# Kernel tuning notes

Measured on AMD Instinct MI355X. Metric: run time of the kernel, lower is better.

## Reference

```python
import jax, jax.numpy as jnp
import numpy as np

B, T, C, F = 2, 2048, 2048, 8192
LN_EPS = 1e-5


def setup_inputs() -> dict:
    key = jax.random.key(0)
    ks = jax.random.split(key, 24)
    rn = lambda k, s, sc=1.0: jax.random.normal(k, s, jnp.float32) * sc
    un = lambda k, s: jax.random.uniform(k, s, jnp.float32)
    inp = {}
    inp['x'] = rn(ks[0], (B, T, C))
    inp['att_shift'] = rn(ks[1], (B, C))
    # wkv_state rows: aa (num), bb (den), pp (running max exponent)
    inp['wkv_state'] = jnp.stack([jnp.zeros((B, C)), jnp.zeros((B, C)),
                                  jnp.full((B, C), -1e38)], axis=1)
    inp['ffn_shift'] = rn(ks[2], (B, C))
    inp['ln1_g'] = jnp.ones(C); inp['ln1_b'] = jnp.zeros(C)
    inp['ln2_g'] = jnp.ones(C); inp['ln2_b'] = jnp.zeros(C)
    inp['tmk'] = un(ks[3], (C,)); inp['tmv'] = un(ks[4], (C,)); inp['tmr'] = un(ks[5], (C,))
    inp['time_decay'] = rn(ks[6], (C,), 0.5)
    inp['time_first'] = rn(ks[7], (C,), 0.5)
    inp['Wk'] = rn(ks[8], (C, C), 0.02); inp['Wv'] = rn(ks[9], (C, C), 0.02)
    inp['Wr'] = rn(ks[10], (C, C), 0.02); inp['Wo'] = rn(ks[11], (C, C), 0.02)
    inp['fmk'] = un(ks[12], (C,)); inp['fmr'] = un(ks[13], (C,))
    inp['Fk'] = rn(ks[14], (C, F), 0.02)
    inp['Fr'] = rn(ks[15], (C, C), 0.02)
    inp['Fv'] = rn(ks[16], (F, C), 0.02)
    return inp


def layer_norm(x, g, b):
    m = jnp.mean(x, axis=-1, keepdims=True)
    v = jnp.mean(jnp.square(x - m), axis=-1, keepdims=True)
    return (x - m) * jax.lax.rsqrt(v + LN_EPS) * g + b


def wkv(w, u, k, v, state):
    # w: -exp(time_decay) [C], u: time_first [C]; k,v: [B,T,C]; state: [B,3,C]
    def step(carry, kv_t):
        aa, bb, pp = carry
        kt, vt = kv_t
        ww = u + kt
        p = jnp.maximum(pp, ww)
        e1 = jnp.exp(pp - p)
        e2 = jnp.exp(ww - p)
        y = (e1 * aa + e2 * vt) / (e1 * bb + e2)
        ww2 = pp + w
        p2 = jnp.maximum(ww2, kt)
        e1b = jnp.exp(ww2 - p2)
        e2b = jnp.exp(kt - p2)
        return (e1b * aa + e2b * vt, e1b * bb + e2b, p2), y
    carry0 = (state[:, 0], state[:, 1], state[:, 2])
    (aa, bb, pp), ys = jax.lax.scan(step, carry0,
                                    (k.transpose(1, 0, 2), v.transpose(1, 0, 2)))
    return ys.transpose(1, 0, 2), jnp.stack([aa, bb, pp], axis=1)


def reference(x, att_shift, wkv_state, ffn_shift, ln1_g, ln1_b, ln2_g, ln2_b,
              tmk, tmv, tmr, time_decay, time_first, Wk, Wv, Wr, Wo,
              fmk, fmr, Fk, Fr, Fv):
    # ---- time-mix (attention) ----
    x1 = layer_norm(x, ln1_g, ln1_b)
    xx = jnp.concatenate([att_shift[:, None, :], x1[:, :-1]], axis=1)
    xk = x1 * tmk + xx * (1.0 - tmk)
    xv = x1 * tmv + xx * (1.0 - tmv)
    xr = x1 * tmr + xx * (1.0 - tmr)
    k = jnp.einsum('btc,cd->btd', xk, Wk)
    v = jnp.einsum('btc,cd->btd', xv, Wv)
    r = jnp.einsum('btc,cd->btd', xr, Wr)
    y, new_wkv = wkv(-jnp.exp(time_decay), time_first, k, v, wkv_state)
    x = x + jnp.einsum('btd,dc->btc', jax.nn.sigmoid(r) * y, Wo)
    # ---- channel-mix (FFN) ----
    x2 = layer_norm(x, ln2_g, ln2_b)
    xx2 = jnp.concatenate([ffn_shift[:, None, :], x2[:, :-1]], axis=1)
    xk2 = x2 * fmk + xx2 * (1.0 - fmk)
    xr2 = x2 * fmr + xx2 * (1.0 - fmr)
    kf = jnp.square(jax.nn.relu(jnp.einsum('btc,cf->btf', xk2, Fk)))
    kv = jnp.einsum('btf,fc->btc', kf, Fv)
    x = x + jax.nn.sigmoid(jnp.einsum('btc,cd->btd', xr2, Fr)) * kv
    return x, x1[:, -1], new_wkv, x2[:, -1]
```

## Files before the change

kernel.cpp:

```cpp
#include <hip/hip_runtime.h>
#include <stdint.h>

#define B_ 2
#define T_ 2048
#define C_ 2048
#define F_ 8192
#define M_ 4096
#define BC_ 4096
#define CHB 16
#define TCH 16
#define LC2 128

typedef __attribute__((ext_vector_type(8))) __bf16 bf16x8;
typedef __attribute__((ext_vector_type(4))) float f32x4;

__device__ __forceinline__ unsigned short f2bf(float f) {
  union { float f; unsigned u; } v; v.f = f;
  unsigned r = v.u + 0x7fffu + ((v.u >> 16) & 1u);
  return (unsigned short)(r >> 16);
}
__device__ __forceinline__ float b2f(unsigned short h) {
  union { unsigned u; float f; } v; v.u = ((unsigned)h) << 16; return v.f;
}

__device__ __forceinline__ void gload16(const void* g, void* l) {
  __builtin_amdgcn_global_load_lds((__attribute__((address_space(1))) void*)g,
                                   (__attribute__((address_space(3))) void*)l,
                                   16, 0, 0);
}

__global__ __launch_bounds__(256) void k_transpose_cast(
    const float* __restrict__ W, unsigned short* __restrict__ WT, int K, int N) {
  __shared__ unsigned short tile[32][33];
  const int n0 = blockIdx.x * 32, k0 = blockIdx.y * 32;
  const int tx = threadIdx.x & 31, ty = threadIdx.x >> 5;
#pragma unroll
  for (int i = 0; i < 4; ++i)
    tile[ty + 8 * i][tx] = f2bf(W[(size_t)(k0 + ty + 8 * i) * N + n0 + tx]);
  __syncthreads();
#pragma unroll
  for (int i = 0; i < 4; ++i)
    WT[(size_t)(n0 + ty + 8 * i) * K + k0 + tx] = tile[tx][ty + 8 * i];
}

__global__ __launch_bounds__(256) void k_layernorm(
    const float* __restrict__ x, const float* __restrict__ g,
    const float* __restrict__ beta, unsigned short* __restrict__ y,
    float* __restrict__ last_out) {
  const int row = blockIdx.x;
  const int t = row & (T_ - 1);
  const int bi = row >> 11;
  const float* xr = x + (size_t)row * C_;
  const int base = threadIdx.x * 8;
  float lv[8];
  {
    float4 a = *(const float4*)(xr + base);
    float4 b = *(const float4*)(xr + base + 4);
    lv[0]=a.x; lv[1]=a.y; lv[2]=a.z; lv[3]=a.w; lv[4]=b.x; lv[5]=b.y; lv[6]=b.z; lv[7]=b.w;
  }
  float s = 0.f, q = 0.f;
#pragma unroll
  for (int j = 0; j < 8; ++j) { s += lv[j]; q += lv[j] * lv[j]; }
#pragma unroll
  for (int o = 32; o > 0; o >>= 1) { s += __shfl_down(s, o); q += __shfl_down(q, o); }
  __shared__ float rs[4], rq[4];
  if ((threadIdx.x & 63) == 0) { rs[threadIdx.x >> 6] = s; rq[threadIdx.x >> 6] = q; }
  __syncthreads();
  s = rs[0] + rs[1] + rs[2] + rs[3];
  q = rq[0] + rq[1] + rq[2] + rq[3];
  const float mean = s * (1.f / C_);
  const float var = q * (1.f / C_) - mean * mean;
  const float inv = 1.f / sqrtf(var + 1e-5f);
  float ov[8];
  unsigned short o8[8];
#pragma unroll
  for (int j = 0; j < 8; ++j) {
    ov[j] = (lv[j] - mean) * inv * g[base + j] + beta[base + j];
    o8[j] = f2bf(ov[j]);
  }
  *(uint4*)(y + (size_t)row * C_ + base) = *(uint4*)o8;
  if (last_out != nullptr && t == T_ - 1) {
    float* lp = last_out + (size_t)bi * C_ + base;
    *(float4*)lp = make_float4(ov[0], ov[1], ov[2], ov[3]);
    *(float4*)(lp + 4) = make_float4(ov[4], ov[5], ov[6], ov[7]);
  }
}

__global__ __launch_bounds__(256) void k_mix3(
    const unsigned short* __restrict__ x1, const float* __restrict__ shift,
    const float* __restrict__ tmk, const float* __restrict__ tmv,
    const float* __restrict__ tmr,
    unsigned short* __restrict__ xk, unsigned short* __restrict__ xv,
    unsigned short* __restrict__ xr) {
  const int row = blockIdx.x;
  const int t = row & (T_ - 1);
  const int bi = row >> 11;
  const int c0 = threadIdx.x * 8;
  const size_t o = (size_t)row * C_ + c0;
  unsigned short cur8[8];
  *(uint4*)cur8 = *(const uint4*)(x1 + o);
  float pv[8];
  if (t == 0) {
    const float* sp = shift + (size_t)bi * C_ + c0;
#pragma unroll
    for (int j = 0; j < 8; ++j) pv[j] = sp[j];
  } else {
    unsigned short p8[8];
    *(uint4*)p8 = *(const uint4*)(x1 + o - C_);
#pragma unroll
    for (int j = 0; j < 8; ++j) pv[j] = b2f(p8[j]);
  }
  unsigned short ok[8], ov[8], orr[8];
#pragma unroll
  for (int j = 0; j < 8; ++j) {
    const float a = b2f(cur8[j]), p = pv[j];
    const float mk = tmk[c0 + j], mv = tmv[c0 + j], mr = tmr[c0 + j];
    ok[j]  = f2bf(a * mk + p * (1.f - mk));
    ov[j]  = f2bf(a * mv + p * (1.f - mv));
    orr[j] = f2bf(a * mr + p * (1.f - mr));
  }
  *(uint4*)(xk + o) = *(uint4*)ok;
  *(uint4*)(xv + o) = *(uint4*)ov;
  *(uint4*)(xr + o) = *(uint4*)orr;
}

__global__ __launch_bounds__(256) void k_mix2(
    const unsigned short* __restrict__ x2, const float* __restrict__ shift,
    const float* __restrict__ fmk, const float* __restrict__ fmr,
    unsigned short* __restrict__ xk2, unsigned short* __restrict__ xr2) {
  const int row = blockIdx.x;
  const int t = row & (T_ - 1);
  const int bi = row >> 11;
  const int c0 = threadIdx.x * 8;
  const size_t o = (size_t)row * C_ + c0;
  unsigned short cur8[8];
  *(uint4*)cur8 = *(const uint4*)(x2 + o);
  float pv[8];
  if (t == 0) {
    const float* sp = shift + (size_t)bi * C_ + c0;
#pragma unroll
    for (int j = 0; j < 8; ++j) pv[j] = sp[j];
  } else {
    unsigned short p8[8];
    *(uint4*)p8 = *(const uint4*)(x2 + o - C_);
#pragma unroll
    for (int j = 0; j < 8; ++j) pv[j] = b2f(p8[j]);
  }
  unsigned short ok[8], orr[8];
#pragma unroll
  for (int j = 0; j < 8; ++j) {
    const float a = b2f(cur8[j]), p = pv[j];
    const float mk = fmk[c0 + j], mr = fmr[c0 + j];
    ok[j]  = f2bf(a * mk + p * (1.f - mk));
    orr[j] = f2bf(a * mr + p * (1.f - mr));
  }
  *(uint4*)(xk2 + o) = *(uint4*)ok;
  *(uint4*)(xr2 + o) = *(uint4*)orr;
}

__global__ __launch_bounds__(256) void k_wkv_blk(
    const float* __restrict__ kk, const float* __restrict__ vv,
    const float* __restrict__ td, const float* __restrict__ tf,
    const float* __restrict__ st, float* __restrict__ y,
    float* __restrict__ out_state) {
  __shared__ float sA[TCH][CHB], sB[TCH][CHB], sP[TCH][CHB];
  const int blk = blockIdx.x;
  const int bi = blk >> 7;
  const int tx = threadIdx.x & 15;
  const int ty = threadIdx.x >> 4;
  const int c = ((blk & 127) * CHB) + tx;
  const float w = -expf(td[c]);
  const float u = tf[c];
  const size_t base = (size_t)bi * T_ * C_ + (size_t)ty * LC2 * C_ + c;
  const float* kp = kk + base;
  const float* vp = vv + base;
  float aa = 0.f, bb = 0.f, pp = -1e38f;
#pragma unroll 8
  for (int i = 0; i < LC2; ++i) {
    const float kt = kp[(size_t)i * C_], vt = vp[(size_t)i * C_];
    const float ww2 = pp + w;
    const float p2 = fmaxf(ww2, kt);
    const float e1b = expf(ww2 - p2), e2b = expf(kt - p2);
    aa = e1b * aa + e2b * vt;
    bb = e1b * bb + e2b;
    pp = p2;
  }
  sA[ty][tx] = aa; sB[ty][tx] = bb; sP[ty][tx] = pp;
  __syncthreads();
  if (ty == 0) {
    const float* s0 = st + (size_t)bi * 3 * C_;
    float ca = s0[c], cb = s0[C_ + c], cp = s0[2 * C_ + c];
    const float wL = w * (float)LC2;
#pragma unroll
    for (int j = 0; j < TCH; ++j) {
      const float a2 = sA[j][tx], b2 = sB[j][tx], p2 = sP[j][tx];
      sA[j][tx] = ca; sB[j][tx] = cb; sP[j][tx] = cp;
      const float pd = cp + wL;
      const float pm = fmaxf(pd, p2);
      const float e1 = expf(pd - pm), e2 = expf(p2 - pm);
      ca = e1 * ca + e2 * a2;
      cb = e1 * cb + e2 * b2;
      cp = pm;
    }
  }
  __syncthreads();
  aa = sA[ty][tx]; bb = sB[ty][tx]; pp = sP[ty][tx];
  float* yp = y + base;
#pragma unroll 4
  for (int i = 0; i < LC2; ++i) {
    const float kt = kp[(size_t)i * C_], vt = vp[(size_t)i * C_];
    const float ww = u + kt;
    const float p = fmaxf(pp, ww);
    const float e1 = expf(pp - p), e2 = expf(ww - p);
    yp[(size_t)i * C_] = (e1 * aa + e2 * vt) / (e1 * bb + e2);
    const float ww2 = pp + w;
    const float p2 = fmaxf(ww2, kt);
    const float e1b = expf(ww2 - p2), e2b = expf(kt - p2);
    aa = e1b * aa + e2b * vt;
    bb = e1b * bb + e2b;
    pp = p2;
  }
  if (ty == TCH - 1) {
    float* ob = out_state + (size_t)bi * 3 * C_;
    ob[c] = aa; ob[C_ + c] = bb; ob[2 * C_ + c] = pp;
  }
}

__global__ __launch_bounds__(256) void k_sry(
    const unsigned short* __restrict__ r, const float* __restrict__ y,
    unsigned short* __restrict__ sry) {
  const int nv = M_ * C_ / 8;
  for (int i = blockIdx.x * 256 + threadIdx.x; i < nv; i += gridDim.x * 256) {
    unsigned short r8[8];
    *(uint4*)r8 = ((const uint4*)r)[i];
    float4 ya = ((const float4*)y)[2 * i], yb = ((const float4*)y)[2 * i + 1];
    const float yv[8] = {ya.x, ya.y, ya.z, ya.w, yb.x, yb.y, yb.z, yb.w};
    unsigned short o8[8];
#pragma unroll
    for (int j = 0; j < 8; ++j) {
      const float s = 1.f / (1.f + expf(-b2f(r8[j])));
      o8[j] = f2bf(s * yv[j]);
    }
    ((uint4*)sry)[i] = *(uint4*)o8;
  }
}

template <int EPI, int SWZ>
__global__ __launch_bounds__(512, 1) void k_gemm8(
    const unsigned short* __restrict__ A, const unsigned short* __restrict__ BT,
    int K, int Nn, void* __restrict__ out,
    const float* __restrict__ aux1, const float* __restrict__ aux2) {
  __shared__ unsigned short lds[73728];
  const int tid = threadIdx.x;
  const int lane = tid & 63;
  const int wid = tid >> 6;
  int mBase, nBase;
  if (SWZ) {
    const int gx = gridDim.x, gy = gridDim.y;
    const int wg = blockIdx.y * gx + blockIdx.x;
    const int per = (gx * gy) >> 3;
    const int p = 31 - __clz(per);
    const int nr = 1 << ((p - 1) >> 1);
    const int mr = per / nr;
    if ((gx % nr) == 0 && (gy % mr) == 0) {
      const int gxr = gx / nr;
      const int xcd = wg & 7, idx = wg >> 3;
      const int rr = xcd / gxr, rc = xcd % gxr;
      mBase = (rr * mr + idx / nr) * 128;
      nBase = (rc * nr + idx % nr) * 256;
    } else {
      int w2 = (wg & 7) * per + (wg >> 3);
      mBase = (w2 / gx) * 128;
      nBase = (w2 % gx) * 256;
    }
  } else {
    mBase = blockIdx.y * 128;
    nBase = blockIdx.x * 256;
  }
  const int wr = (wid >> 2) * 64;
  const int wc = (wid & 3) * 64;
  const int r16 = lane & 15, kq = lane >> 4;
  const int lrow = lane >> 3;
  const int lslot = (lane & 7) ^ lrow;
  const int xsw = r16 & 7;
  f32x4 acc[4][4] = {};

  const unsigned short* gA0 = A  + (size_t)(mBase + 0   + wid * 8 + lrow) * K + lslot * 8;
  const unsigned short* gA1 = A  + (size_t)(mBase + 64  + wid * 8 + lrow) * K + lslot * 8;
  const unsigned short* gB0 = BT + (size_t)(nBase + 0   + wid * 8 + lrow) * K + lslot * 8;
  const unsigned short* gB1 = BT + (size_t)(nBase + 64  + wid * 8 + lrow) * K + lslot * 8;
  const unsigned short* gB2 = BT + (size_t)(nBase + 128 + wid * 8 + lrow) * K + lslot * 8;
  const unsigned short* gB3 = BT + (size_t)(nBase + 192 + wid * 8 + lrow) * K + lslot * 8;
  const int wof = wid * 512;
  int aoff[4][2], boff[4][2];
#pragma unroll
  for (int m = 0; m < 4; ++m)
#pragma unroll
    for (int s = 0; s < 2; ++s)
      aoff[m][s] = (wr + m * 16 + r16) * 64 + (((s * 4 + kq) ^ xsw) * 8);
#pragma unroll
  for (int n = 0; n < 4; ++n)
#pragma unroll
    for (int s = 0; s < 2; ++s)
      boff[n][s] = 8192 + (wc + n * 16 + r16) * 64 + (((s * 4 + kq) ^ xsw) * 8);

  const int nt = K >> 6;
  gload16(gA0, &lds[0 + wof]);
  gload16(gA1, &lds[4096 + wof]);
  gload16(gB0, &lds[8192 + wof]);
  gload16(gB1, &lds[12288 + wof]);
  gload16(gB2, &lds[16384 + wof]);
  gload16(gB3, &lds[20480 + wof]);
  gload16(gA0 + 64, &lds[24576 + 0 + wof]);
  gload16(gA1 + 64, &lds[24576 + 4096 + wof]);
  gload16(gB0 + 64, &lds[24576 + 8192 + wof]);
  gload16(gB1 + 64, &lds[24576 + 12288 + wof]);
  gload16(gB2 + 64, &lds[24576 + 16384 + wof]);
  gload16(gB3 + 64, &lds[24576 + 20480 + wof]);
  asm volatile("s_waitcnt vmcnt(6)" ::: "memory");
  asm volatile("s_barrier" ::: "memory");

  int cb = 0;
  for (int t = 0; t < nt; ++t) {
    const int nb = (cb >= 1) ? cb - 1 : 2;
    const int ca = cb * 24576;
    const int nba = nb * 24576;
    const int kb2 = (t + 2) << 6;
    const bool pf = (t + 2) < nt;
    if (pf) {
      gload16(gA0 + kb2, &lds[nba + 0 + wof]);
      gload16(gA1 + kb2, &lds[nba + 4096 + wof]);
      gload16(gB0 + kb2, &lds[nba + 8192 + wof]);
      gload16(gB1 + kb2, &lds[nba + 12288 + wof]);
      gload16(gB2 + kb2, &lds[nba + 16384 + wof]);
      gload16(gB3 + kb2, &lds[nba + 20480 + wof]);
    }
    bf16x8 af[4][2], bq[4][2];
#pragma unroll
    for (int m = 0; m < 4; ++m)
#pragma unroll
      for (int s = 0; s < 2; ++s)
        af[m][s] = *(const bf16x8*)&lds[ca + aoff[m][s]];
#pragma unroll
    for (int n = 0; n < 4; ++n)
#pragma unroll
      for (int s = 0; s < 2; ++s)
        bq[n][s] = *(const bf16x8*)&lds[ca + boff[n][s]];
    __builtin_amdgcn_s_setprio(1);
#pragma unroll
    for (int m = 0; m < 4; ++m)
#pragma unroll
      for (int n = 0; n < 4; ++n)
#pragma unroll
        for (int s = 0; s < 2; ++s)
          acc[m][n] = __builtin_amdgcn_mfma_f32_16x16x32_bf16(
              af[m][s], bq[n][s], acc[m][n], 0, 0, 0);
    __builtin_amdgcn_s_setprio(0);
    if (pf) {
      asm volatile("s_waitcnt vmcnt(6)" ::: "memory");
    } else if (t + 1 < nt) {
      asm volatile("s_waitcnt vmcnt(0)" ::: "memory");
    }
    asm volatile("s_barrier" ::: "memory");
    cb = (cb == 2) ? 0 : cb + 1;
  }

  const int c0 = kq * 4;
#pragma unroll
  for (int m = 0; m < 4; ++m) {
#pragma unroll
    for (int n = 0; n < 4; ++n) {
      const int col = nBase + wc + n * 16 + r16;
#pragma unroll
      for (int e = 0; e < 4; ++e) {
        const int rowg = mBase + wr + m * 16 + c0 + e;
        const size_t idx = (size_t)rowg * Nn + col;
        const float va = acc[m][n][e];
        if (EPI == 0) {
          ((float*)out)[idx] = va;
        } else if (EPI == 1) {
          const float t = va > 0.f ? va : 0.f;
          ((unsigned short*)out)[idx] = f2bf(t * t);
        } else if (EPI == 2) {
          ((float*)out)[idx] = aux1[idx] + va;
        } else if (EPI == 3) {
          const float s = 1.f / (1.f + expf(-va));
          ((float*)out)[idx] = aux1[idx] + s * aux2[idx];
        } else {
          ((unsigned short*)out)[idx] = f2bf(va);
        }
      }
    }
  }
}

extern "C" void kernel_launch(void* const* d_in, const int* in_sizes, int n_in,
                              void* d_out, int out_size, void* d_ws, size_t ws_size,
                              hipStream_t stream) {
  const float* x          = (const float*)d_in[0];
  const float* att_shift  = (const float*)d_in[1];
  const float* wkv_state  = (const float*)d_in[2];
  const float* ffn_shift  = (const float*)d_in[3];
  const float* ln1_g = (const float*)d_in[4];
  const float* ln1_b = (const float*)d_in[5];
  const float* ln2_g = (const float*)d_in[6];
  const float* ln2_b = (const float*)d_in[7];
  const float* tmk = (const float*)d_in[8];
  const float* tmv = (const float*)d_in[9];
  const float* tmr = (const float*)d_in[10];
  const float* time_decay = (const float*)d_in[11];
  const float* time_first = (const float*)d_in[12];
  const float* Wk = (const float*)d_in[13];
  const float* Wv = (const float*)d_in[14];
  const float* Wr = (const float*)d_in[15];
  const float* Wo = (const float*)d_in[16];
  const float* fmk = (const float*)d_in[17];
  const float* fmr = (const float*)d_in[18];
  const float* Fk = (const float*)d_in[19];
  const float* Fr = (const float*)d_in[20];
  const float* Fv = (const float*)d_in[21];

  const size_t MB = 1ull << 20;
  char* ws = (char*)d_ws;
  if (ws_size < 176 * MB) return;

  unsigned short* Wslot = (unsigned short*)(ws);
  float*          kBuf  = (float*)(ws + 32 * MB);
  float*          vBuf  = (float*)(ws + 64 * MB);
  float*          yBuf  = (float*)(ws + 96 * MB);
  unsigned short* h1    = (unsigned short*)(ws + 128 * MB);
  unsigned short* h2    = (unsigned short*)(ws + 144 * MB);
  unsigned short* h3    = (unsigned short*)(ws + 160 * MB);
  unsigned short* xrT   = (unsigned short*)kBuf;
  unsigned short* kf    = (unsigned short*)kBuf;
  float*          kv    = (float*)h1;

  float* outb    = (float*)d_out;
  float* x1_last = outb + (size_t)M_ * C_;
  float* wkv_out = x1_last + (size_t)B_ * C_;
  float* x2_last = wkv_out + (size_t)B_ * 3 * C_;

  const dim3 gCC(C_ / 32, C_ / 32);
  const dim3 gC8(C_ / 256, M_ / 128);
  const dim3 gF8(F_ / 256, M_ / 128);

  k_layernorm<<<M_, 256, 0, stream>>>(x, ln1_g, ln1_b, h1, x1_last);
  k_mix3<<<M_, 256, 0, stream>>>(h1, att_shift, tmk, tmv, tmr, h2, h3, xrT);
  k_transpose_cast<<<gCC, 256, 0, stream>>>(Wr, Wslot, C_, C_);
  k_gemm8<4,1><<<gC8, 512, 0, stream>>>(xrT, Wslot, C_, C_, h1, nullptr, nullptr);
  k_transpose_cast<<<gCC, 256, 0, stream>>>(Wk, Wslot, C_, C_);
  k_gemm8<0,1><<<gC8, 512, 0, stream>>>(h2, Wslot, C_, C_, kBuf, nullptr, nullptr);
  k_transpose_cast<<<gCC, 256, 0, stream>>>(Wv, Wslot, C_, C_);
  k_gemm8<0,1><<<gC8, 512, 0, stream>>>(h3, Wslot, C_, C_, vBuf, nullptr, nullptr);
  k_wkv_blk<<<dim3(BC_ / CHB), 256, 0, stream>>>(kBuf, vBuf, time_decay, time_first,
                                                 wkv_state, yBuf, wkv_out);
  k_sry<<<1024, 256, 0, stream>>>(h1, yBuf, h2);
  k_transpose_cast<<<gCC, 256, 0, stream>>>(Wo, Wslot, C_, C_);
  k_gemm8<2,1><<<gC8, 512, 0, stream>>>(h2, Wslot, C_, C_, yBuf, x, nullptr);

  k_layernorm<<<M_, 256, 0, stream>>>(yBuf, ln2_g, ln2_b, h1, x2_last);
  k_mix2<<<M_, 256, 0, stream>>>(h1, ffn_shift, fmk, fmr, h2, h3);
  k_transpose_cast<<<dim3(F_ / 32, C_ / 32), 256, 0, stream>>>(Fk, Wslot, C_, F_);
  k_gemm8<1,1><<<gF8, 512, 0, stream>>>(h2, Wslot, C_, F_, kf, nullptr, nullptr);
  k_transpose_cast<<<dim3(C_ / 32, F_ / 32), 256, 0, stream>>>(Fv, Wslot, F_, C_);
  k_gemm8<0,1><<<gC8, 512, 0, stream>>>(kf, Wslot, F_, C_, kv, nullptr, nullptr);
  k_transpose_cast<<<gCC, 256, 0, stream>>>(Fr, Wslot, C_, C_);
  k_gemm8<3,1><<<gC8, 512, 0, stream>>>(h3, Wslot, C_, C_, d_out, yBuf, kv);
}
```

Before: 679.0 us.

## Add 256x256-tile GEMM kernel for the FFN key projection

Adds a new GEMM kernel with 256x256 output tiles, a 64-wide K step, double-buffered LDS (128 KB) and an XCD-aware block swizzle. It is used only for the large C->F key projection, replacing the 128x256 tile kernel. The bigger tile roughly doubles arithmetic intensity per loaded byte and halves the number of workgroups. The cost is one workgroup per CU with high register pressure (128 accumulator floats per lane), which limits latency hiding.

```diff
diff --git a/kernel.cpp b/kernel.cpp
--- a/kernel.cpp
+++ b/kernel.cpp
@@ -394,6 +394,136 @@
   }
 }
 
+template <int EPI, int SWZ>
+__global__ __launch_bounds__(512, 1) void k_gemm256(
+    const unsigned short* __restrict__ A, const unsigned short* __restrict__ BT,
+    int K, int Nn, void* __restrict__ out,
+    const float* __restrict__ aux1, const float* __restrict__ aux2) {
+  __shared__ unsigned short lds[65536];
+  const int tid = threadIdx.x;
+  const int lane = tid & 63;
+  const int wid = tid >> 6;
+  int mBase, nBase;
+  if (SWZ) {
+    const int gx = gridDim.x, gy = gridDim.y;
+    const int wg = blockIdx.y * gx + blockIdx.x;
+    const int per = (gx * gy) >> 3;
+    const int p = 31 - __clz(per);
+    const int nr = 1 << (p >> 1);
+    const int mr = per / nr;
+    if ((gx % nr) == 0 && (gy % mr) == 0) {
+      const int gxr = gx / nr;
+      const int xcd = wg & 7, idx = wg >> 3;
+      const int rr = xcd / gxr, rc = xcd % gxr;
+      mBase = (rr * mr + idx / nr) * 256;
+      nBase = (rc * nr + idx % nr) * 256;
+    } else {
+      int w2 = (wg & 7) * per + (wg >> 3);
+      mBase = (w2 / gx) * 256;
+      nBase = (w2 % gx) * 256;
+    }
+  } else {
+    mBase = blockIdx.y * 256;
+    nBase = blockIdx.x * 256;
+  }
+  const int wr = (wid >> 2) * 128;
+  const int wc = (wid & 3) * 64;
+  const int r16 = lane & 15, kq = lane >> 4;
+  const int lrow = lane >> 3;
+  const int lslot = (lane & 7) ^ lrow;
+  const int xsw = r16 & 7;
+  f32x4 acc[8][4] = {};
+
+  const unsigned short* gA[4];
+  const unsigned short* gB[4];
+#pragma unroll
+  for (int j = 0; j < 4; ++j) {
+    gA[j] = A  + (size_t)(mBase + j * 64 + wid * 8 + lrow) * K + lslot * 8;
+    gB[j] = BT + (size_t)(nBase + j * 64 + wid * 8 + lrow) * K + lslot * 8;
+  }
+  const int wof = wid * 512;
+
+  const int nt = K >> 6;
+#pragma unroll
+  for (int j = 0; j < 4; ++j) {
+    gload16(gA[j], &lds[j * 4096 + wof]);
+    gload16(gB[j], &lds[16384 + j * 4096 + wof]);
+  }
+  asm volatile("s_waitcnt vmcnt(0)" ::: "memory");
+  asm volatile("s_barrier" ::: "memory");
+
+  for (int t = 0; t < nt; ++t) {
+    const int ca = (t & 1) * 32768;
+    const int nba = ((t + 1) & 1) * 32768;
+    const int kb1 = (t + 1) << 6;
+    const bool pf = (t + 1) < nt;
+    if (pf) {
+#pragma unroll
+      for (int j = 0; j < 4; ++j) {
+        gload16(gA[j] + kb1, &lds[nba + j * 4096 + wof]);
+        gload16(gB[j] + kb1, &lds[nba + 16384 + j * 4096 + wof]);
+      }
+    }
+    bf16x8 bq[4][2];
+#pragma unroll
+    for (int n = 0; n < 4; ++n)
+#pragma unroll
+      for (int s = 0; s < 2; ++s)
+        bq[n][s] = *(const bf16x8*)&lds[ca + 16384 + (wc + n * 16 + r16) * 64 +
+                                        (((s * 4 + kq) ^ xsw) * 8)];
+#pragma unroll
+    for (int qm = 0; qm < 2; ++qm) {
+      bf16x8 af[4][2];
+#pragma unroll
+      for (int m = 0; m < 4; ++m)
+#pragma unroll
+        for (int s = 0; s < 2; ++s)
+          af[m][s] = *(const bf16x8*)&lds[ca + (wr + (qm * 4 + m) * 16 + r16) * 64 +
+                                          (((s * 4 + kq) ^ xsw) * 8)];
+      __builtin_amdgcn_s_setprio(1);
+#pragma unroll
+      for (int m = 0; m < 4; ++m)
+#pragma unroll
+        for (int n = 0; n < 4; ++n)
+#pragma unroll
+          for (int s = 0; s < 2; ++s)
+            acc[qm * 4 + m][n] = __builtin_amdgcn_mfma_f32_16x16x32_bf16(
+                af[m][s], bq[n][s], acc[qm * 4 + m][n], 0, 0, 0);
+      __builtin_amdgcn_s_setprio(0);
+    }
+    if (pf) asm volatile("s_waitcnt vmcnt(0)" ::: "memory");
+    asm volatile("s_barrier" ::: "memory");
+  }
+
+  const int c0 = kq * 4;
+#pragma unroll
+  for (int m = 0; m < 8; ++m) {
+#pragma unroll
+    for (int n = 0; n < 4; ++n) {
+      const int col = nBase + wc + n * 16 + r16;
+#pragma unroll
+      for (int e = 0; e < 4; ++e) {
+        const int rowg = mBase + wr + m * 16 + c0 + e;
+        const size_t idx = (size_t)rowg * Nn + col;
+        const float va = acc[m][n][e];
+        if (EPI == 0) {
+          ((float*)out)[idx] = va;
+        } else if (EPI == 1) {
+          const float t = va > 0.f ? va : 0.f;
+          ((unsigned short*)out)[idx] = f2bf(t * t);
+        } else if (EPI == 2) {
+          ((float*)out)[idx] = aux1[idx] + va;
+        } else if (EPI == 3) {
+          const float s = 1.f / (1.f + expf(-va));
+          ((float*)out)[idx] = aux1[idx] + s * aux2[idx];
+        } else {
+          ((unsigned short*)out)[idx] = f2bf(va);
+        }
+      }
+    }
+  }
+}
+
 extern "C" void kernel_launch(void* const* d_in, const int* in_sizes, int n_in,
                               void* d_out, int out_size, void* d_ws, size_t ws_size,
                               hipStream_t stream) {
@@ -442,7 +572,7 @@
 
   const dim3 gCC(C_ / 32, C_ / 32);
   const dim3 gC8(C_ / 256, M_ / 128);
-  const dim3 gF8(F_ / 256, M_ / 128);
+  const dim3 gF256(F_ / 256, M_ / 256);
 
   k_layernorm<<<M_, 256, 0, stream>>>(x, ln1_g, ln1_b, h1, x1_last);
   k_mix3<<<M_, 256, 0, stream>>>(h1, att_shift, tmk, tmv, tmr, h2, h3, xrT);
@@ -461,7 +591,7 @@
   k_layernorm<<<M_, 256, 0, stream>>>(yBuf, ln2_g, ln2_b, h1, x2_last);
   k_mix2<<<M_, 256, 0, stream>>>(h1, ffn_shift, fmk, fmr, h2, h3);
   k_transpose_cast<<<dim3(F_ / 32, C_ / 32), 256, 0, stream>>>(Fk, Wslot, C_, F_);
-  k_gemm8<1,1><<<gF8, 512, 0, stream>>>(h2, Wslot, C_, F_, kf, nullptr, nullptr);
+  k_gemm256<1,1><<<gF256, 512, 0, stream>>>(h2, Wslot, C_, F_, kf, nullptr, nullptr);
   k_transpose_cast<<<dim3(C_ / 32, F_ / 32), 256, 0, stream>>>(Fv, Wslot, F_, C_);
   k_gemm8<0,1><<<gC8, 512, 0, stream>>>(kf, Wslot, F_, C_, kv, nullptr, nullptr);
   k_transpose_cast<<<gCC, 256, 0, stream>>>(Fr, Wslot, C_, C_);
```

New measurement: 644.2 us. 1.05x faster.
